# Kernel tuning notes

Measured on AMD Instinct MI355X. Metric: run time of the kernel, lower is better.

The kernel has to match this reference:

```python
import jax, jax.numpy as jnp
import numpy as np

N_NODES = 100000
N_EDGES = 3200000
IN_DIM = 64
HID = 64


def setup_inputs() -> dict:
    key = jax.random.key(0)
    ks = jax.random.split(key, 12)
    x = jax.random.normal(ks[0], (N_NODES, IN_DIM), dtype=jnp.float32)
    edge_index = jax.random.randint(ks[1], (2, N_EDGES), 0, N_NODES, dtype=jnp.int64)
    tau = jax.random.uniform(ks[2], (N_NODES, 1), dtype=jnp.float32)
    d1 = IN_DIM + 1  # augmented feature dim
    s1 = 1.0 / np.sqrt(d1)
    s2 = 1.0 / np.sqrt(HID)
    # SAGEConv: out = lin_l(mean_aggr) + lin_r(x); bias lives in lin_l. Weights stored [in, out].
    W1l = jax.random.uniform(ks[3], (d1, HID), jnp.float32, -s1, s1)
    b1l = jax.random.uniform(ks[4], (HID,), jnp.float32, -s1, s1)
    W1r = jax.random.uniform(ks[5], (d1, HID), jnp.float32, -s1, s1)
    W2l = jax.random.uniform(ks[6], (HID, HID), jnp.float32, -s2, s2)
    b2l = jax.random.uniform(ks[7], (HID,), jnp.float32, -s2, s2)
    W2r = jax.random.uniform(ks[8], (HID, HID), jnp.float32, -s2, s2)
    Wfc = jax.random.uniform(ks[9], (HID, 1), jnp.float32, -s2, s2)
    bfc = jax.random.uniform(ks[10], (1,), jnp.float32, -s2, s2)
    return {"x": x, "edge_index": edge_index, "tau": tau,
            "W1l": W1l, "b1l": b1l, "W1r": W1r,
            "W2l": W2l, "b2l": b2l, "W2r": W2r,
            "Wfc": Wfc, "bfc": bfc}


def _sage_conv(x, src, dst, Wl, bl, Wr, n_nodes):
    # mean aggregation of source-node features onto target nodes
    summed = jax.ops.segment_sum(x[src], dst, num_segments=n_nodes)  # [N, d]
    deg = jax.ops.segment_sum(jnp.ones(src.shape[0], x.dtype), dst, num_segments=n_nodes)
    mean = summed / jnp.maximum(deg, 1.0)[:, None]
    return mean @ Wl + bl + x @ Wr


def reference(x, edge_index, tau, W1l, b1l, W1r, W2l, b2l, W2r, Wfc, bfc):
    src, dst = edge_index[0], edge_index[1]
    n = x.shape[0]
    h = jnp.concatenate([x, tau], axis=1)  # augment_features: append tau column
    h = jax.nn.relu(_sage_conv(h, src, dst, W1l, b1l, W1r, n))
    h = jax.nn.relu(_sage_conv(h, src, dst, W2l, b2l, W2r, n))
    return h @ Wfc + bfc  # [N, 1]
```

## Files before the change

### kernel.cpp

```cpp
#include <hip/hip_runtime.h>
#include <hip/hip_bf16.h>
#include <hip/hip_fp16.h>
#include <hip/hip_fp8.h>


#define BSH 7
#define NBKT 782
#define NBLK 512
#define PER 6250
#define CAP 6144
#define ABLK 512

typedef _Float16 half8 __attribute__((ext_vector_type(8)));
typedef float floatx4 __attribute__((ext_vector_type(4)));
typedef float floatx2 __attribute__((ext_vector_type(2)));

struct h4s { __half2 lo, hi; };

#if __has_builtin(__builtin_amdgcn_cvt_pk_f32_fp8)
template <bool HI>
__device__ __forceinline__ float2 f8x2_to_f2(int v) {
    floatx2 r = __builtin_amdgcn_cvt_pk_f32_fp8(v, HI);
    return make_float2(r.x, r.y);
}
#else
template <bool HI>
__device__ __forceinline__ float2 f8x2_to_f2(int v) {
    unsigned short u = HI ? (unsigned short)(((unsigned)v) >> 16)
                          : (unsigned short)(v & 0xFFFF);
    __half2_raw r = __hip_cvt_fp8x2_to_halfraw2((__hip_fp8x2_storage_t)u, __HIP_E4M3);
    return __half22float2(*(__half2*)&r);
}
#endif

#if __has_builtin(__builtin_amdgcn_cvt_pk_fp8_f32)
__device__ __forceinline__ unsigned f4_to_f8x4(float a, float b, float c, float d) {
    int lo = __builtin_amdgcn_cvt_pk_fp8_f32(a, b, 0, false);
    return (unsigned)__builtin_amdgcn_cvt_pk_fp8_f32(c, d, lo, true);
}
__device__ __forceinline__ unsigned char f_to_f8(float a) {
    return (unsigned char)(__builtin_amdgcn_cvt_pk_fp8_f32(a, a, 0, false) & 0xFF);
}
#else
__device__ __forceinline__ unsigned f4_to_f8x4(float a, float b, float c, float d) {
    unsigned lo = (unsigned)__hip_cvt_float2_to_fp8x2(make_float2(a, b), __HIP_SATFINITE, __HIP_E4M3);
    unsigned hi = (unsigned)__hip_cvt_float2_to_fp8x2(make_float2(c, d), __HIP_SATFINITE, __HIP_E4M3);
    return lo | (hi << 16);
}
__device__ __forceinline__ unsigned char f_to_f8(float a) {
    return (unsigned char)__hip_cvt_float_to_fp8(a, __HIP_SATFINITE, __HIP_E4M3);
}
#endif

__global__ __launch_bounds__(256) void k_histprep(
    const int* __restrict__ dst, int* __restrict__ histT, int E,
    const float* __restrict__ x, __half* __restrict__ xh,
    unsigned char* __restrict__ xf8, int n4,
    const float* __restrict__ W1l, const float* __restrict__ W1r,
    const float* __restrict__ W2l, const float* __restrict__ W2r,
    __half* __restrict__ wbuf1, __half* __restrict__ wbuf2) {
    if (blockIdx.x < NBLK) {
        __shared__ int h[NBKT];
        for (int i = threadIdx.x; i < NBKT; i += 256) h[i] = 0;
        __syncthreads();
        int lo = blockIdx.x * PER;
        int hi = lo + PER; if (hi > E) hi = E;
        for (int e = lo + threadIdx.x; e < hi; e += 256)
            atomicAdd(&h[dst[e] >> BSH], 1);
        __syncthreads();
        for (int k = threadIdx.x; k < NBKT; k += 256)
            histT[k * NBLK + blockIdx.x] = h[k];
    } else if (blockIdx.x < NBLK + 9) {
        int idx = (blockIdx.x - NBLK) * 256 + threadIdx.x;
        if (idx < 1280) {
            int lane = idx & 63;
            int nt = (idx >> 6) & 3;
            int kstep = idx >> 8;
            int col = nt * 16 + (lane & 15);
            int kbase = kstep * 32 + (lane >> 4) * 8;
#pragma unroll
            for (int j = 0; j < 8; ++j) {
                int k = kbase + j;
                float v;
                if (k < 64)        v = W1l[k * 64 + col];
                else if (k < 128)  v = W1r[(k - 64) * 64 + col];
                else if (k == 128) v = W1l[64 * 64 + col];
                else if (k == 129) v = W1r[64 * 64 + col];
                else v = 0.f;
                wbuf1[(size_t)idx * 8 + j] = __float2half(v);
            }
        } else if (idx < 1280 + 1024) {
            int i2 = idx - 1280;
            int lane = i2 & 63;
            int nt = (i2 >> 6) & 3;
            int kstep = i2 >> 8;
            int col = nt * 16 + (lane & 15);
            int kbase = kstep * 32 + (lane >> 4) * 8;
#pragma unroll
            for (int j = 0; j < 8; ++j) {
                int k = kbase + j;
                float v = (k < 64) ? W2l[k * 64 + col] : W2r[(k - 64) * 64 + col];
                wbuf2[(size_t)i2 * 8 + j] = __float2half(v);
            }
        }
    } else {
        int i = (blockIdx.x - NBLK - 9) * 256 + threadIdx.x;
        if (i < n4) {
            float4 v = ((const float4*)x)[i];
            ((__half2*)xh)[2 * i]     = __floats2half2_rn(v.x, v.y);
            ((__half2*)xh)[2 * i + 1] = __floats2half2_rn(v.z, v.w);
            ((unsigned*)xf8)[i] = f4_to_f8x4(v.x, v.y, v.z, v.w);
        }
    }
}


__global__ __launch_bounds__(NBLK) void k_scanblk(int* __restrict__ histT,
                                                  int* __restrict__ btot) {
    __shared__ int s[NBLK];
    int k = blockIdx.x, t = threadIdx.x;
    int v = histT[k * NBLK + t];
    s[t] = v;
    __syncthreads();
    for (int off = 1; off < NBLK; off <<= 1) {
        int u = (t >= off) ? s[t - off] : 0;
        __syncthreads();
        s[t] += u;
        __syncthreads();
    }
    histT[k * NBLK + t] = s[t] - v;
    if (t == NBLK - 1) btot[k] = s[t];
}

__global__ __launch_bounds__(1024) void k_scanbkt(const int* __restrict__ btot,
                                                  int* __restrict__ bstart) {
    __shared__ int s[1024];
    int t = threadIdx.x;
    int v = (t < NBKT) ? btot[t] : 0;
    s[t] = v;
    __syncthreads();
    for (int off = 1; off < 1024; off <<= 1) {
        int u = (t >= off) ? s[t - off] : 0;
        __syncthreads();
        s[t] += u;
        __syncthreads();
    }
    if (t < NBKT) bstart[t] = s[t] - v;
    if (t == NBKT - 1) bstart[NBKT] = s[t];
}

__global__ __launch_bounds__(256) void k_scatter(const int* __restrict__ src,
                                                 const int* __restrict__ dst,
                                                 const int* __restrict__ histT,
                                                 const int* __restrict__ bstart,
                                                 int* __restrict__ binned, int E) {
    __shared__ int sorted[PER];
    __shared__ int lstart[NBKT + 1];
    __shared__ int cur[NBKT];
    __shared__ int gst[NBKT];
    __shared__ int tsum[256];
    int b = blockIdx.x, t = threadIdx.x;
    int base = b * PER;
    int blen = E - base; if (blen > PER) blen = PER;

    for (int k = t; k < NBKT; k += 256) lstart[k] = 0;
    __syncthreads();
    for (int e = base + t; e < base + blen; e += 256)
        atomicAdd(&lstart[dst[e] >> BSH], 1);
    __syncthreads();
    int c0 = 0;
    int i0 = t * 4;
#pragma unroll
    for (int j = 0; j < 4; ++j)
        if (i0 + j < NBKT) c0 += lstart[i0 + j];
    tsum[t] = c0;
    __syncthreads();
    for (int off = 1; off < 256; off <<= 1) {
        int u = (t >= off) ? tsum[t - off] : 0;
        __syncthreads();
        tsum[t] += u;
        __syncthreads();
    }
    int running = tsum[t] - c0;
    __syncthreads();
#pragma unroll
    for (int j = 0; j < 4; ++j) {
        int i = i0 + j;
        if (i < NBKT) {
            int v = lstart[i];
            lstart[i] = running;
            running += v;
        }
    }
    __syncthreads();
    if (t == 0) lstart[NBKT] = blen;
    for (int k = t; k < NBKT; k += 256) {
        cur[k] = lstart[k];
        gst[k] = bstart[k] + histT[k * NBLK + b];
    }
    __syncthreads();
    for (int e = base + t; e < base + blen; e += 256) {
        int d = dst[e], s = src[e];
        int pos = atomicAdd(&cur[d >> BSH], 1);
        sorted[pos] = (s << BSH) | (d & ((1 << BSH) - 1));
    }
    __syncthreads();
    int qw = t >> 4, ql = t & 15;
    for (int k = qw; k < NBKT; k += 16) {
        int st = lstart[k];
        int ln = lstart[k + 1] - st;
        int gd = gst[k];
        for (int i = ql; i < ln; i += 16)
            binned[gd + i] = sorted[st + i];
    }
}


__global__ __launch_bounds__(ABLK) void k_aggrb1(
    const int* __restrict__ binned, const int* __restrict__ bstart,
    const unsigned char* __restrict__ xf8, const float* __restrict__ tau,
    __half* __restrict__ zm1, __half* __restrict__ mt1, int N) {
    __shared__ int cidx[CAP];
    __shared__ int cnt[128], s[128], cur[128];
    int k = blockIdx.x, t = threadIdx.x;
    int lo = bstart[k], hi = bstart[k + 1];
    if (t < 128) cnt[t] = 0;
    __syncthreads();
    for (int e = lo + t; e < hi; e += ABLK)
        atomicAdd(&cnt[binned[e] & 127], 1);
    __syncthreads();
    if (t < 128) s[t] = cnt[t];
    __syncthreads();
    for (int off = 1; off < 128; off <<= 1) {
        int u = 0;
        if (t < 128 && t >= off) u = s[t - off];
        __syncthreads();
        if (t < 128) s[t] += u;
        __syncthreads();
    }
    if (t < 128) cur[t] = s[t] - cnt[t];
    __syncthreads();
    for (int e = lo + t; e < hi; e += ABLK) {
        int p = binned[e];
        int pos = atomicAdd(&cur[p & 127], 1);
        if (pos < CAP) cidx[pos] = p >> BSH;
    }
    __syncthreads();

    int lane = t & 63;
    int q = lane >> 4;
    int c = lane & 15;
    int qb = lane & 48;
    unsigned cb = (unsigned)(c << 2);
    const char* xb = (const char*)xf8;

    for (int p = (t >> 6); p < 32; p += (ABLK / 64)) {
        int ld = (p << 2) + q;
        int node = (k << BSH) + ld;
        int d = cnt[ld];
        int startL = cur[ld] - d;
        int dm = d;
        dm = max(dm, __shfl_xor(dm, 16, 64));
        dm = max(dm, __shfl_xor(dm, 32, 64));
        float4 A0 = {0.f, 0.f, 0.f, 0.f}, A1 = A0, A2 = A0, A3 = A0;
        float sumtau = 0.f;
        for (int base = 0; base < dm; base += 16) {
            int n = d - base;
            n = (n < 0) ? 0 : (n > 16 ? 16 : n);
            int nmax = dm - base; if (nmax > 16) nmax = 16;
            int sidx = 0;
            if (c < n) {
                int ii = startL + base + c;
                if (ii >= CAP) ii = 0;
                sidx = cidx[ii];
                sumtau += tau[sidx];
            }
            int j = 0;
            for (; j + 4 <= nmax; j += 4) {
                int i0 = __builtin_amdgcn_ds_bpermute((qb + j + 0) << 2, sidx);
                int i1 = __builtin_amdgcn_ds_bpermute((qb + j + 1) << 2, sidx);
                int i2 = __builtin_amdgcn_ds_bpermute((qb + j + 2) << 2, sidx);
                int i3 = __builtin_amdgcn_ds_bpermute((qb + j + 3) << 2, sidx);
                int r0 = *(const int*)(xb + (((unsigned)i0 << 6) + cb));
                int r1 = *(const int*)(xb + (((unsigned)i1 << 6) + cb));
                int r2 = *(const int*)(xb + (((unsigned)i2 << 6) + cb));
                int r3 = *(const int*)(xb + (((unsigned)i3 << 6) + cb));
                float2 l0 = f8x2_to_f2<false>(r0), h0 = f8x2_to_f2<true>(r0);
                float2 l1 = f8x2_to_f2<false>(r1), h1v = f8x2_to_f2<true>(r1);
                float2 l2 = f8x2_to_f2<false>(r2), h2v = f8x2_to_f2<true>(r2);
                float2 l3 = f8x2_to_f2<false>(r3), h3v = f8x2_to_f2<true>(r3);
                if (j + 0 < n) { A0.x += l0.x; A0.y += l0.y; A0.z += h0.x; A0.w += h0.y; }
                if (j + 1 < n) { A1.x += l1.x; A1.y += l1.y; A1.z += h1v.x; A1.w += h1v.y; }
                if (j + 2 < n) { A2.x += l2.x; A2.y += l2.y; A2.z += h2v.x; A2.w += h2v.y; }
                if (j + 3 < n) { A3.x += l3.x; A3.y += l3.y; A3.z += h3v.x; A3.w += h3v.y; }
            }
            for (; j < nmax; ++j) {
                int i0 = __builtin_amdgcn_ds_bpermute((qb + j) << 2, sidx);
                int r0 = *(const int*)(xb + (((unsigned)i0 << 6) + cb));
                float2 l0 = f8x2_to_f2<false>(r0), h0 = f8x2_to_f2<true>(r0);
                if (j < n) { A0.x += l0.x; A0.y += l0.y; A0.z += h0.x; A0.w += h0.y; }
            }
        }
        float4 A;
        A.x = (A0.x + A1.x) + (A2.x + A3.x);
        A.y = (A0.y + A1.y) + (A2.y + A3.y);
        A.z = (A0.z + A1.z) + (A2.z + A3.z);
        A.w = (A0.w + A1.w) + (A2.w + A3.w);
#pragma unroll
        for (int off = 8; off > 0; off >>= 1) sumtau += __shfl_xor(sumtau, off, 64);

        float inv = 1.f / fmaxf((float)d, 1.f);
        if (node < N) {
            h4s o;
            o.lo = __floats2half2_rn(A.x * inv, A.y * inv);
            o.hi = __floats2half2_rn(A.z * inv, A.w * inv);
            *(h4s*)(zm1 + (size_t)node * 64 + (c << 2)) = o;
            if (c == 0) mt1[node] = __float2half(sumtau * inv);
        }
    }
}

__global__ __launch_bounds__(ABLK) void k_aggrb2(
    const int* __restrict__ binned, const int* __restrict__ bstart,
    const unsigned char* __restrict__ h1f8, __half* __restrict__ zm2, int N) {
    __shared__ int cidx[CAP];
    __shared__ int cnt[128], s[128], cur[128];
    int k = blockIdx.x, t = threadIdx.x;
    int lo = bstart[k], hi = bstart[k + 1];
    if (t < 128) cnt[t] = 0;
    __syncthreads();
    for (int e = lo + t; e < hi; e += ABLK)
        atomicAdd(&cnt[binned[e] & 127], 1);
    __syncthreads();
    if (t < 128) s[t] = cnt[t];
    __syncthreads();
    for (int off = 1; off < 128; off <<= 1) {
        int u = 0;
        if (t < 128 && t >= off) u = s[t - off];
        __syncthreads();
        if (t < 128) s[t] += u;
        __syncthreads();
    }
    if (t < 128) cur[t] = s[t] - cnt[t];
    __syncthreads();
    for (int e = lo + t; e < hi; e += ABLK) {
        int p = binned[e];
        int pos = atomicAdd(&cur[p & 127], 1);
        if (pos < CAP) cidx[pos] = p >> BSH;
    }
    __syncthreads();

    int lane = t & 63;
    int q = lane >> 4;
    int c = lane & 15;
    int qb = lane & 48;
    unsigned cb = (unsigned)(c << 2);
    const char* hb = (const char*)h1f8;

    for (int p = (t >> 6); p < 32; p += (ABLK / 64)) {
        int ld = (p << 2) + q;
        int node = (k << BSH) + ld;
        int d = cnt[ld];
        int startL = cur[ld] - d;
        int dm = d;
        dm = max(dm, __shfl_xor(dm, 16, 64));
        dm = max(dm, __shfl_xor(dm, 32, 64));
        float4 A0 = {0.f, 0.f, 0.f, 0.f}, A1 = A0, A2 = A0, A3 = A0;
        for (int base = 0; base < dm; base += 16) {
            int n = d - base;
            n = (n < 0) ? 0 : (n > 16 ? 16 : n);
            int nmax = dm - base; if (nmax > 16) nmax = 16;
            int sidx = 0;
            if (c < n) {
                int ii = startL + base + c;
                if (ii >= CAP) ii = 0;
                sidx = cidx[ii];
            }
            int j = 0;
            for (; j + 4 <= nmax; j += 4) {
                int i0 = __builtin_amdgcn_ds_bpermute((qb + j + 0) << 2, sidx);
                int i1 = __builtin_amdgcn_ds_bpermute((qb + j + 1) << 2, sidx);
                int i2 = __builtin_amdgcn_ds_bpermute((qb + j + 2) << 2, sidx);
                int i3 = __builtin_amdgcn_ds_bpermute((qb + j + 3) << 2, sidx);
                int r0 = *(const int*)(hb + (((unsigned)i0 << 6) + cb));
                int r1 = *(const int*)(hb + (((unsigned)i1 << 6) + cb));
                int r2 = *(const int*)(hb + (((unsigned)i2 << 6) + cb));
                int r3 = *(const int*)(hb + (((unsigned)i3 << 6) + cb));
                float2 l0 = f8x2_to_f2<false>(r0), h0 = f8x2_to_f2<true>(r0);
                float2 l1 = f8x2_to_f2<false>(r1), h1v = f8x2_to_f2<true>(r1);
                float2 l2 = f8x2_to_f2<false>(r2), h2v = f8x2_to_f2<true>(r2);
                float2 l3 = f8x2_to_f2<false>(r3), h3v = f8x2_to_f2<true>(r3);
                if (j + 0 < n) { A0.x += l0.x; A0.y += l0.y; A0.z += h0.x; A0.w += h0.y; }
                if (j + 1 < n) { A1.x += l1.x; A1.y += l1.y; A1.z += h1v.x; A1.w += h1v.y; }
                if (j + 2 < n) { A2.x += l2.x; A2.y += l2.y; A2.z += h2v.x; A2.w += h2v.y; }
                if (j + 3 < n) { A3.x += l3.x; A3.y += l3.y; A3.z += h3v.x; A3.w += h3v.y; }
            }
            for (; j < nmax; ++j) {
                int i0 = __builtin_amdgcn_ds_bpermute((qb + j) << 2, sidx);
                int r0 = *(const int*)(hb + (((unsigned)i0 << 6) + cb));
                float2 l0 = f8x2_to_f2<false>(r0), h0 = f8x2_to_f2<true>(r0);
                if (j < n) { A0.x += l0.x; A0.y += l0.y; A0.z += h0.x; A0.w += h0.y; }
            }
        }
        float4 A;
        A.x = (A0.x + A1.x) + (A2.x + A3.x);
        A.y = (A0.y + A1.y) + (A2.y + A3.y);
        A.z = (A0.z + A1.z) + (A2.z + A3.z);
        A.w = (A0.w + A1.w) + (A2.w + A3.w);
        float inv = 1.f / fmaxf((float)d, 1.f);
        if (node < N) {
            h4s o;
            o.lo = __floats2half2_rn(A.x * inv, A.y * inv);
            o.hi = __floats2half2_rn(A.z * inv, A.w * inv);
            *(h4s*)(zm2 + (size_t)node * 64 + (c << 2)) = o;
        }
    }
}


__global__ __launch_bounds__(256) void k_gemm1(
    const __half* __restrict__ zm1, const __half* __restrict__ mt1,
    const __half* __restrict__ xh, const float* __restrict__ tau,
    const __half* __restrict__ wbuf1, const float* __restrict__ b1l,
    __half* __restrict__ h1, unsigned char* __restrict__ h1f8, int ntiles) {
    int tile = blockIdx.x * 4 + (threadIdx.x >> 6);
    if (tile >= ntiles) return;
    int lane = threadIdx.x & 63;
    int sub = lane & 15;
    int quad = lane >> 4;
    int row = tile * 16 + sub;

    floatx4 acc0 = {0.f, 0.f, 0.f, 0.f};
    floatx4 acc1 = {0.f, 0.f, 0.f, 0.f};
    floatx4 acc2 = {0.f, 0.f, 0.f, 0.f};
    floatx4 acc3 = {0.f, 0.f, 0.f, 0.f};

    const _Float16* zrow = (const _Float16*)zm1 + (size_t)row * 64 + quad * 8;
    const _Float16* xrow = (const _Float16*)xh + (size_t)row * 64 + quad * 8;
    const _Float16* wb = (const _Float16*)wbuf1 + (size_t)lane * 8;

    half8 amat[5];
    amat[0] = *(const half8*)(zrow);
    amat[1] = *(const half8*)(zrow + 32);
    amat[2] = *(const half8*)(xrow);
    amat[3] = *(const half8*)(xrow + 32);
    half8 a4 = {0, 0, 0, 0, 0, 0, 0, 0};
    if (quad == 0) {
        a4[0] = ((const _Float16*)mt1)[row];
        a4[1] = (_Float16)tau[row];
    }
    amat[4] = a4;

#pragma unroll
    for (int ks = 0; ks < 5; ++ks) {
        half8 a = amat[ks];
        half8 b0 = *(const half8*)(wb + (size_t)(ks * 4 + 0) * 512);
        half8 b1 = *(const half8*)(wb + (size_t)(ks * 4 + 1) * 512);
        half8 b2 = *(const half8*)(wb + (size_t)(ks * 4 + 2) * 512);
        half8 b3 = *(const half8*)(wb + (size_t)(ks * 4 + 3) * 512);
        acc0 = __builtin_amdgcn_mfma_f32_16x16x32_f16(a, b0, acc0, 0, 0, 0);
        acc1 = __builtin_amdgcn_mfma_f32_16x16x32_f16(a, b1, acc1, 0, 0, 0);
        acc2 = __builtin_amdgcn_mfma_f32_16x16x32_f16(a, b2, acc2, 0, 0, 0);
        acc3 = __builtin_amdgcn_mfma_f32_16x16x32_f16(a, b3, acc3, 0, 0, 0);
    }
    float bv0 = b1l[sub], bv1 = b1l[16 + sub], bv2 = b1l[32 + sub], bv3 = b1l[48 + sub];
#pragma unroll
    for (int reg = 0; reg < 4; ++reg) {
        int r = quad * 4 + reg;
        float v0 = fmaxf(acc0[reg] + bv0, 0.f);
        float v1 = fmaxf(acc1[reg] + bv1, 0.f);
        float v2 = fmaxf(acc2[reg] + bv2, 0.f);
        float v3 = fmaxf(acc3[reg] + bv3, 0.f);
        __half* orow = h1 + (size_t)(tile * 16 + r) * 64;
        orow[sub]      = __float2half(v0);
        orow[16 + sub] = __float2half(v1);
        orow[32 + sub] = __float2half(v2);
        orow[48 + sub] = __float2half(v3);
        unsigned char* orow8 = h1f8 + (size_t)(tile * 16 + r) * 64;
        orow8[sub]      = f_to_f8(v0);
        orow8[16 + sub] = f_to_f8(v1);
        orow8[32 + sub] = f_to_f8(v2);
        orow8[48 + sub] = f_to_f8(v3);
    }
}

__global__ __launch_bounds__(256) void k_gemm2(
    const __half* __restrict__ zm2, const __half* __restrict__ h1,
    const __half* __restrict__ wbuf2, const float* __restrict__ b2l,
    const float* __restrict__ Wfc, const float* __restrict__ bfc,
    float* __restrict__ out, int ntiles) {
    int tile = blockIdx.x * 4 + (threadIdx.x >> 6);
    if (tile >= ntiles) return;
    int lane = threadIdx.x & 63;
    int sub = lane & 15;
    int quad = lane >> 4;
    int row = tile * 16 + sub;

    floatx4 acc0 = {0.f, 0.f, 0.f, 0.f};
    floatx4 acc1 = {0.f, 0.f, 0.f, 0.f};
    floatx4 acc2 = {0.f, 0.f, 0.f, 0.f};
    floatx4 acc3 = {0.f, 0.f, 0.f, 0.f};

    const _Float16* zrow = (const _Float16*)zm2 + (size_t)row * 64 + quad * 8;
    const _Float16* hrow = (const _Float16*)h1 + (size_t)row * 64 + quad * 8;
    const _Float16* wb = (const _Float16*)wbuf2 + (size_t)lane * 8;

    half8 amat[4];
    amat[0] = *(const half8*)(zrow);
    amat[1] = *(const half8*)(zrow + 32);
    amat[2] = *(const half8*)(hrow);
    amat[3] = *(const half8*)(hrow + 32);

#pragma unroll
    for (int ks = 0; ks < 4; ++ks) {
        half8 a = amat[ks];
        half8 b0 = *(const half8*)(wb + (size_t)(ks * 4 + 0) * 512);
        half8 b1 = *(const half8*)(wb + (size_t)(ks * 4 + 1) * 512);
        half8 b2 = *(const half8*)(wb + (size_t)(ks * 4 + 2) * 512);
        half8 b3 = *(const half8*)(wb + (size_t)(ks * 4 + 3) * 512);
        acc0 = __builtin_amdgcn_mfma_f32_16x16x32_f16(a, b0, acc0, 0, 0, 0);
        acc1 = __builtin_amdgcn_mfma_f32_16x16x32_f16(a, b1, acc1, 0, 0, 0);
        acc2 = __builtin_amdgcn_mfma_f32_16x16x32_f16(a, b2, acc2, 0, 0, 0);
        acc3 = __builtin_amdgcn_mfma_f32_16x16x32_f16(a, b3, acc3, 0, 0, 0);
    }
    float bb0 = b2l[sub], bb1 = b2l[16 + sub], bb2 = b2l[32 + sub], bb3 = b2l[48 + sub];
    float wv0 = Wfc[sub], wv1 = Wfc[16 + sub], wv2 = Wfc[32 + sub], wv3 = Wfc[48 + sub];
    float p[4];
#pragma unroll
    for (int reg = 0; reg < 4; ++reg) {
        p[reg] = fmaxf(acc0[reg] + bb0, 0.f) * wv0
               + fmaxf(acc1[reg] + bb1, 0.f) * wv1
               + fmaxf(acc2[reg] + bb2, 0.f) * wv2
               + fmaxf(acc3[reg] + bb3, 0.f) * wv3;
    }
#pragma unroll
    for (int m = 1; m <= 8; m <<= 1) {
#pragma unroll
        for (int reg = 0; reg < 4; ++reg) p[reg] += __shfl_xor(p[reg], m, 64);
    }
    if (sub == 0) {
        float b0 = bfc[0];
#pragma unroll
        for (int reg = 0; reg < 4; ++reg)
            out[tile * 16 + quad * 4 + reg] = p[reg] + b0;
    }
}

extern "C" void kernel_launch(void* const* d_in, const int* in_sizes, int n_in,
                              void* d_out, int out_size, void* d_ws, size_t ws_size,
                              hipStream_t stream) {
    const float* x   = (const float*)d_in[0];
    const int*   ei  = (const int*)d_in[1];
    const float* tau = (const float*)d_in[2];
    const float* W1l = (const float*)d_in[3];
    const float* b1l = (const float*)d_in[4];
    const float* W1r = (const float*)d_in[5];
    const float* W2l = (const float*)d_in[6];
    const float* b2l = (const float*)d_in[7];
    const float* W2r = (const float*)d_in[8];
    const float* Wfc = (const float*)d_in[9];
    const float* bfc = (const float*)d_in[10];
    float* out = (float*)d_out;

    const int N = in_sizes[0] / 64;
    const int E = in_sizes[1] / 2;
    const int* src = ei;
    const int* dst = ei + E;

    char* w = (char*)d_ws;
    auto take = [&](size_t b) { char* p = w; w += (b + 255) & ~(size_t)255; return p; };
    int*           histT  = (int*)take((size_t)NBKT * NBLK * 4);
    int*           btot   = (int*)take((size_t)NBKT * 4);
    int*           bstart = (int*)take((size_t)(NBKT + 1) * 4);
    int*           binned = (int*)take((size_t)E * 4);
    __half*        xh     = (__half*)take((size_t)N * 64 * 2);
    unsigned char* xf8    = (unsigned char*)take((size_t)N * 64);
    __half*        h1     = (__half*)take((size_t)N * 64 * 2);
    unsigned char* h1f8   = (unsigned char*)take((size_t)N * 64);
    __half*        zm1    = (__half*)take((size_t)N * 64 * 2);
    __half*        mt1    = (__half*)take((size_t)N * 2);
    __half*        zm2    = (__half*)take((size_t)N * 64 * 2);
    __half*        wbuf1  = (__half*)take(1280 * 8 * 2);
    __half*        wbuf2  = (__half*)take(1024 * 8 * 2);

    int n4 = N * 16;
    int hpblocks = NBLK + 9 + (n4 + 255) / 256;
    int ntiles = N / 16;
    int gblocks = (ntiles + 3) / 4;

    k_histprep<<<hpblocks, 256, 0, stream>>>(dst, histT, E, x, xh, xf8, n4,
                                             W1l, W1r, W2l, W2r, wbuf1, wbuf2);
    k_scanblk <<<NBKT, NBLK, 0, stream>>>(histT, btot);
    k_scanbkt <<<1, 1024, 0, stream>>>(btot, bstart);
    k_scatter <<<NBLK, 256, 0, stream>>>(src, dst, histT, bstart, binned, E);
    k_aggrb1  <<<NBKT, ABLK, 0, stream>>>(binned, bstart, xf8, tau, zm1, mt1, N);
    k_gemm1   <<<gblocks, 256, 0, stream>>>(zm1, mt1, xh, tau, wbuf1, b1l, h1, h1f8, ntiles);
    k_aggrb2  <<<NBKT, ABLK, 0, stream>>>(binned, bstart, h1f8, zm2, N);
    k_gemm2   <<<gblocks, 256, 0, stream>>>(zm2, h1, wbuf2, b2l, Wfc, bfc, out, ntiles);
}
```

Measured before the change: 268.7 us.

## Gather 16-byte fp8 rows per lane and reduce partial sums with shuffles

Both aggregation kernels now split each 16-lane node group into 4 edge slots by 4 column chunks. Each lane loads 16 bytes of a neighbor row instead of 4 bytes, so a node's 16 neighbors are fetched in four wide loads rather than sixteen narrow ones. Partial sums are combined with cross-lane xor shuffles and each lane writes its own 4-column slice. This cuts load instruction count and raises bytes per load, at the cost of extra shuffle reductions and more live registers.

```diff
diff --git a/kernel.cpp b/kernel.cpp
--- a/kernel.cpp
+++ b/kernel.cpp
@@ -251,7 +251,10 @@
     int q = lane >> 4;
     int c = lane & 15;
     int qb = lane & 48;
-    unsigned cb = (unsigned)(c << 2);
+    int g = c & 3;
+    int ch = c >> 2;
+    unsigned cb = (unsigned)(ch << 4);
+    int bpl = (qb + g) << 2;
     const char* xb = (const char*)xf8;
 
     for (int p = (t >> 6); p < 32; p += (ABLK / 64)) {
@@ -268,6 +271,7 @@
             int n = d - base;
             n = (n < 0) ? 0 : (n > 16 ? 16 : n);
             int nmax = dm - base; if (nmax > 16) nmax = 16;
+            int ng = (nmax + 3) >> 2;
             int sidx = 0;
             if (c < n) {
                 int ii = startL + base + c;
@@ -275,46 +279,57 @@
                 sidx = cidx[ii];
                 sumtau += tau[sidx];
             }
-            int j = 0;
-            for (; j + 4 <= nmax; j += 4) {
-                int i0 = __builtin_amdgcn_ds_bpermute((qb + j + 0) << 2, sidx);
-                int i1 = __builtin_amdgcn_ds_bpermute((qb + j + 1) << 2, sidx);
-                int i2 = __builtin_amdgcn_ds_bpermute((qb + j + 2) << 2, sidx);
-                int i3 = __builtin_amdgcn_ds_bpermute((qb + j + 3) << 2, sidx);
-                int r0 = *(const int*)(xb + (((unsigned)i0 << 6) + cb));
-                int r1 = *(const int*)(xb + (((unsigned)i1 << 6) + cb));
-                int r2 = *(const int*)(xb + (((unsigned)i2 << 6) + cb));
-                int r3 = *(const int*)(xb + (((unsigned)i3 << 6) + cb));
-                float2 l0 = f8x2_to_f2<false>(r0), h0 = f8x2_to_f2<true>(r0);
-                float2 l1 = f8x2_to_f2<false>(r1), h1v = f8x2_to_f2<true>(r1);
-                float2 l2 = f8x2_to_f2<false>(r2), h2v = f8x2_to_f2<true>(r2);
-                float2 l3 = f8x2_to_f2<false>(r3), h3v = f8x2_to_f2<true>(r3);
-                if (j + 0 < n) { A0.x += l0.x; A0.y += l0.y; A0.z += h0.x; A0.w += h0.y; }
-                if (j + 1 < n) { A1.x += l1.x; A1.y += l1.y; A1.z += h1v.x; A1.w += h1v.y; }
-                if (j + 2 < n) { A2.x += l2.x; A2.y += l2.y; A2.z += h2v.x; A2.w += h2v.y; }
-                if (j + 3 < n) { A3.x += l3.x; A3.y += l3.y; A3.z += h3v.x; A3.w += h3v.y; }
-            }
-            for (; j < nmax; ++j) {
-                int i0 = __builtin_amdgcn_ds_bpermute((qb + j) << 2, sidx);
-                int r0 = *(const int*)(xb + (((unsigned)i0 << 6) + cb));
-                float2 l0 = f8x2_to_f2<false>(r0), h0 = f8x2_to_f2<true>(r0);
-                if (j < n) { A0.x += l0.x; A0.y += l0.y; A0.z += h0.x; A0.w += h0.y; }
-            }
-        }
-        float4 A;
-        A.x = (A0.x + A1.x) + (A2.x + A3.x);
-        A.y = (A0.y + A1.y) + (A2.y + A3.y);
-        A.z = (A0.z + A1.z) + (A2.z + A3.z);
-        A.w = (A0.w + A1.w) + (A2.w + A3.w);
+            int4 r0, r1, r2, r3;
+            int i0 = __builtin_amdgcn_ds_bpermute(bpl, sidx);
+            r0 = *(const int4*)(xb + (((unsigned)i0 << 6) + cb));
+            if (ng > 1) {
+                int i1 = __builtin_amdgcn_ds_bpermute(bpl + 16, sidx);
+                r1 = *(const int4*)(xb + (((unsigned)i1 << 6) + cb));
+            }
+            if (ng > 2) {
+                int i2 = __builtin_amdgcn_ds_bpermute(bpl + 32, sidx);
+                r2 = *(const int4*)(xb + (((unsigned)i2 << 6) + cb));
+            }
+            if (ng > 3) {
+                int i3 = __builtin_amdgcn_ds_bpermute(bpl + 48, sidx);
+                r3 = *(const int4*)(xb + (((unsigned)i3 << 6) + cb));
+            }
+            auto accum = [&](const int4& r) {
+                float2 l0 = f8x2_to_f2<false>(r.x), h0 = f8x2_to_f2<true>(r.x);
+                float2 l1 = f8x2_to_f2<false>(r.y), h1v = f8x2_to_f2<true>(r.y);
+                float2 l2 = f8x2_to_f2<false>(r.z), h2v = f8x2_to_f2<true>(r.z);
+                float2 l3 = f8x2_to_f2<false>(r.w), h3v = f8x2_to_f2<true>(r.w);
+                A0.x += l0.x; A0.y += l0.y; A0.z += h0.x; A0.w += h0.y;
+                A1.x += l1.x; A1.y += l1.y; A1.z += h1v.x; A1.w += h1v.y;
+                A2.x += l2.x; A2.y += l2.y; A2.z += h2v.x; A2.w += h2v.y;
+                A3.x += l3.x; A3.y += l3.y; A3.z += h3v.x; A3.w += h3v.y;
+            };
+            if (g < n)                accum(r0);
+            if (ng > 1 && 4 + g < n)  accum(r1);
+            if (ng > 2 && 8 + g < n)  accum(r2);
+            if (ng > 3 && 12 + g < n) accum(r3);
+        }
+#pragma unroll
+        for (int off = 1; off <= 2; off <<= 1) {
+            A0.x += __shfl_xor(A0.x, off, 64); A0.y += __shfl_xor(A0.y, off, 64);
+            A0.z += __shfl_xor(A0.z, off, 64); A0.w += __shfl_xor(A0.w, off, 64);
+            A1.x += __shfl_xor(A1.x, off, 64); A1.y += __shfl_xor(A1.y, off, 64);
+            A1.z += __shfl_xor(A1.z, off, 64); A1.w += __shfl_xor(A1.w, off, 64);
+            A2.x += __shfl_xor(A2.x, off, 64); A2.y += __shfl_xor(A2.y, off, 64);
+            A2.z += __shfl_xor(A2.z, off, 64); A2.w += __shfl_xor(A2.w, off, 64);
+            A3.x += __shfl_xor(A3.x, off, 64); A3.y += __shfl_xor(A3.y, off, 64);
+            A3.z += __shfl_xor(A3.z, off, 64); A3.w += __shfl_xor(A3.w, off, 64);
+        }
 #pragma unroll
         for (int off = 8; off > 0; off >>= 1) sumtau += __shfl_xor(sumtau, off, 64);
 
         float inv = 1.f / fmaxf((float)d, 1.f);
         if (node < N) {
+            float4 Aw = (g == 0) ? A0 : ((g == 1) ? A1 : ((g == 2) ? A2 : A3));
             h4s o;
-            o.lo = __floats2half2_rn(A.x * inv, A.y * inv);
-            o.hi = __floats2half2_rn(A.z * inv, A.w * inv);
-            *(h4s*)(zm1 + (size_t)node * 64 + (c << 2)) = o;
+            o.lo = __floats2half2_rn(Aw.x * inv, Aw.y * inv);
+            o.hi = __floats2half2_rn(Aw.z * inv, Aw.w * inv);
+            *(h4s*)(zm1 + (size_t)node * 64 + (ch << 4) + (g << 2)) = o;
             if (c == 0) mt1[node] = __float2half(sumtau * inv);
         }
     }
@@ -354,7 +369,10 @@
     int q = lane >> 4;
     int c = lane & 15;
     int qb = lane & 48;
-    unsigned cb = (unsigned)(c << 2);
+    int g = c & 3;
+    int ch = c >> 2;
+    unsigned cb = (unsigned)(ch << 4);
+    int bpl = (qb + g) << 2;
     const char* hb = (const char*)h1f8;
 
     for (int p = (t >> 6); p < 32; p += (ABLK / 64)) {
@@ -370,49 +388,61 @@
             int n = d - base;
             n = (n < 0) ? 0 : (n > 16 ? 16 : n);
             int nmax = dm - base; if (nmax > 16) nmax = 16;
+            int ng = (nmax + 3) >> 2;
             int sidx = 0;
             if (c < n) {
                 int ii = startL + base + c;
                 if (ii >= CAP) ii = 0;
                 sidx = cidx[ii];
             }
-            int j = 0;
-            for (; j + 4 <= nmax; j += 4) {
-                int i0 = __builtin_amdgcn_ds_bpermute((qb + j + 0) << 2, sidx);
-                int i1 = __builtin_amdgcn_ds_bpermute((qb + j + 1) << 2, sidx);
-                int i2 = __builtin_amdgcn_ds_bpermute((qb + j + 2) << 2, sidx);
-                int i3 = __builtin_amdgcn_ds_bpermute((qb + j + 3) << 2, sidx);
-                int r0 = *(const int*)(hb + (((unsigned)i0 << 6) + cb));
-                int r1 = *(const int*)(hb + (((unsigned)i1 << 6) + cb));
-                int r2 = *(const int*)(hb + (((unsigned)i2 << 6) + cb));
-                int r3 = *(const int*)(hb + (((unsigned)i3 << 6) + cb));
-                float2 l0 = f8x2_to_f2<false>(r0), h0 = f8x2_to_f2<true>(r0);
-                float2 l1 = f8x2_to_f2<false>(r1), h1v = f8x2_to_f2<true>(r1);
-                float2 l2 = f8x2_to_f2<false>(r2), h2v = f8x2_to_f2<true>(r2);
-                float2 l3 = f8x2_to_f2<false>(r3), h3v = f8x2_to_f2<true>(r3);
-                if (j + 0 < n) { A0.x += l0.x; A0.y += l0.y; A0.z += h0.x; A0.w += h0.y; }
-                if (j + 1 < n) { A1.x += l1.x; A1.y += l1.y; A1.z += h1v.x; A1.w += h1v.y; }
-                if (j + 2 < n) { A2.x += l2.x; A2.y += l2.y; A2.z += h2v.x; A2.w += h2v.y; }
-                if (j + 3 < n) { A3.x += l3.x; A3.y += l3.y; A3.z += h3v.x; A3.w += h3v.y; }
-            }
-            for (; j < nmax; ++j) {
-                int i0 = __builtin_amdgcn_ds_bpermute((qb + j) << 2, sidx);
-                int r0 = *(const int*)(hb + (((unsigned)i0 << 6) + cb));
-                float2 l0 = f8x2_to_f2<false>(r0), h0 = f8x2_to_f2<true>(r0);
-                if (j < n) { A0.x += l0.x; A0.y += l0.y; A0.z += h0.x; A0.w += h0.y; }
-            }
-        }
-        float4 A;
-        A.x = (A0.x + A1.x) + (A2.x + A3.x);
-        A.y = (A0.y + A1.y) + (A2.y + A3.y);
-        A.z = (A0.z + A1.z) + (A2.z + A3.z);
-        A.w = (A0.w + A1.w) + (A2.w + A3.w);
+            int4 r0, r1, r2, r3;
+            int i0 = __builtin_amdgcn_ds_bpermute(bpl, sidx);
+            r0 = *(const int4*)(hb + (((unsigned)i0 << 6) + cb));
+            if (ng > 1) {
+                int i1 = __builtin_amdgcn_ds_bpermute(bpl + 16, sidx);
+                r1 = *(const int4*)(hb + (((unsigned)i1 << 6) + cb));
+            }
+            if (ng > 2) {
+                int i2 = __builtin_amdgcn_ds_bpermute(bpl + 32, sidx);
+                r2 = *(const int4*)(hb + (((unsigned)i2 << 6) + cb));
+            }
+            if (ng > 3) {
+                int i3 = __builtin_amdgcn_ds_bpermute(bpl + 48, sidx);
+                r3 = *(const int4*)(hb + (((unsigned)i3 << 6) + cb));
+            }
+            auto accum = [&](const int4& r) {
+                float2 l0 = f8x2_to_f2<false>(r.x), h0 = f8x2_to_f2<true>(r.x);
+                float2 l1 = f8x2_to_f2<false>(r.y), h1v = f8x2_to_f2<true>(r.y);
+                float2 l2 = f8x2_to_f2<false>(r.z), h2v = f8x2_to_f2<true>(r.z);
+                float2 l3 = f8x2_to_f2<false>(r.w), h3v = f8x2_to_f2<true>(r.w);
+                A0.x += l0.x; A0.y += l0.y; A0.z += h0.x; A0.w += h0.y;
+                A1.x += l1.x; A1.y += l1.y; A1.z += h1v.x; A1.w += h1v.y;
+                A2.x += l2.x; A2.y += l2.y; A2.z += h2v.x; A2.w += h2v.y;
+                A3.x += l3.x; A3.y += l3.y; A3.z += h3v.x; A3.w += h3v.y;
+            };
+            if (g < n)                accum(r0);
+            if (ng > 1 && 4 + g < n)  accum(r1);
+            if (ng > 2 && 8 + g < n)  accum(r2);
+            if (ng > 3 && 12 + g < n) accum(r3);
+        }
+#pragma unroll
+        for (int off = 1; off <= 2; off <<= 1) {
+            A0.x += __shfl_xor(A0.x, off, 64); A0.y += __shfl_xor(A0.y, off, 64);
+            A0.z += __shfl_xor(A0.z, off, 64); A0.w += __shfl_xor(A0.w, off, 64);
+            A1.x += __shfl_xor(A1.x, off, 64); A1.y += __shfl_xor(A1.y, off, 64);
+            A1.z += __shfl_xor(A1.z, off, 64); A1.w += __shfl_xor(A1.w, off, 64);
+            A2.x += __shfl_xor(A2.x, off, 64); A2.y += __shfl_xor(A2.y, off, 64);
+            A2.z += __shfl_xor(A2.z, off, 64); A2.w += __shfl_xor(A2.w, off, 64);
+            A3.x += __shfl_xor(A3.x, off, 64); A3.y += __shfl_xor(A3.y, off, 64);
+            A3.z += __shfl_xor(A3.z, off, 64); A3.w += __shfl_xor(A3.w, off, 64);
+        }
         float inv = 1.f / fmaxf((float)d, 1.f);
         if (node < N) {
+            float4 Aw = (g == 0) ? A0 : ((g == 1) ? A1 : ((g == 2) ? A2 : A3));
             h4s o;
-            o.lo = __floats2half2_rn(A.x * inv, A.y * inv);
-            o.hi = __floats2half2_rn(A.z * inv, A.w * inv);
-            *(h4s*)(zm2 + (size_t)node * 64 + (c << 2)) = o;
+            o.lo = __floats2half2_rn(Aw.x * inv, Aw.y * inv);
+            o.hi = __floats2half2_rn(Aw.z * inv, Aw.w * inv);
+            *(h4s*)(zm2 + (size_t)node * 64 + (ch << 4) + (g << 2)) = o;
         }
     }
 }
```

After: 276.8 us. 3.0% more time.
